# Performance work log

Measured on AMD Instinct MI355X. Metric: run time of the kernel, lower is better.

The kernel has to match this reference:

```python
import jax, jax.numpy as jnp
import numpy as np

B, P, N, H = 8, 12, 5000, 8
E = 50000
NB = 8
TD0, TD1 = 16, 64
MAX_STEPS = 500


def _proj(x, w1, b1, w2, b2):
    # Projection: Linear -> ReLU -> Linear
    return jax.nn.relu(x @ w1 + b1) @ w2 + b2


def _ln(x, w, b, eps=1e-5):
    # LayerNorm over last two dims [N, H] with affine params [N, H]
    m = jnp.mean(x, axis=(-2, -1), keepdims=True)
    v = jnp.mean((x - m) ** 2, axis=(-2, -1), keepdims=True)
    return (x - m) * jax.lax.rsqrt(v + eps) * w + b


def _time_table():
    # DiffTimeEmbedding buffer: [MAX_STEPS, 2*TD0]
    steps = jnp.arange(MAX_STEPS, dtype=jnp.float32)[:, None]
    dims = jnp.arange(TD0, dtype=jnp.float32)[None, :]
    e = steps * 10.0 ** (dims * 4.0 / TD0)
    return jnp.concatenate([jnp.sin(e), jnp.cos(e)], axis=1)


def setup_inputs() -> dict:
    key = jax.random.key(0)
    ks = jax.random.split(key, 40)
    rn = lambda k, s, sc=0.1: jax.random.normal(k, s, jnp.float32) * sc
    return {
        'x': jax.random.normal(ks[0], (B, P, N), jnp.float32),
        'cond': jax.random.normal(ks[1], (B, P, N, H), jnp.float32),
        'pos': jax.random.normal(ks[2], (N, H), jnp.float32),
        'time': jax.random.randint(ks[3], (B,), 0, MAX_STEPS),
        'edge_index': jax.random.randint(ks[4], (2, E), 0, N),
        'te_w1': rn(ks[5], (2 * TD0, TD1)), 'te_b1': rn(ks[6], (TD1,)),
        'te_w2': rn(ks[7], (TD1, TD1)), 'te_b2': rn(ks[8], (TD1,)),
        'in_w1': rn(ks[9], (1, H)), 'in_b1': rn(ks[10], (H,)),
        'in_w2': rn(ks[11], (H, H)), 'in_b2': rn(ks[12], (H,)),
        'pos_w1': rn(ks[13], (H, H)), 'pos_b1': rn(ks[14], (H,)),
        'pos_w2': rn(ks[15], (H, H)), 'pos_b2': rn(ks[16], (H,)),
        'attn': jax.random.normal(ks[17], (NB + 1, 1), jnp.float32),
        'bt_w1': rn(ks[18], (NB, TD1, H)), 'bt_b1': rn(ks[19], (NB, H)),
        'bt_w2': rn(ks[20], (NB, H, H)), 'bt_b2': rn(ks[21], (NB, H)),
        'bc_w1': rn(ks[22], (NB, H, H)), 'bc_b1': rn(ks[23], (NB, H)),
        'bc_w2': rn(ks[24], (NB, H, H)), 'bc_b2': rn(ks[25], (NB, H)),
        'gn_w': 1.0 + rn(ks[26], (NB, N, H), 0.05), 'gn_b': rn(ks[27], (NB, N, H), 0.05),
        'tn_w': 1.0 + rn(ks[28], (NB, N, H), 0.05), 'tn_b': rn(ks[29], (NB, N, H), 0.05),
        'cv_w': rn(ks[30], (NB, P, P)), 'cv_b': rn(ks[31], (NB, P)),
        'out_w1': rn(ks[32], (H, H)), 'out_b1': rn(ks[33], (H,)),
        'out_w2': rn(ks[34], (H, 1)), 'out_b2': rn(ks[35], (1,)),
    }


def _forward(x, cond, pos, te_w1, te_b1, te_w2, te_b2, in_w1, in_b1, in_w2, in_b2,
             pos_w1, pos_b1, pos_w2, pos_b2, attn, bt_w1, bt_b1, bt_w2, bt_b2,
             bc_w1, bc_b1, bc_w2, bc_b2, gn_w, gn_b, tn_w, tn_b, cv_w, cv_b,
             out_w1, out_b1, out_w2, out_b2, time, edge_index):
    # diffusion-time embedding -> [B, TD1]
    te = _time_table()[time]
    te = jax.nn.silu(te @ te_w1 + te_b1)
    te = jax.nn.silu(te @ te_w2 + te_b2)
    # input + positional projection -> [B, P, N, H]
    h = _proj(x[..., None], in_w1, in_b1, in_w2, in_b2)
    h = h + _proj(pos, pos_w1, pos_b1, pos_w2, pos_b2)
    # LGConv symmetric GCN norm (no self loops), shared across blocks
    src, dst = edge_index[0], edge_index[1]
    deg = jnp.zeros((N,), h.dtype).at[dst].add(1.0)
    dinv = jnp.where(deg > 0, 1.0 / jnp.sqrt(jnp.where(deg > 0, deg, 1.0)), 0.0)
    enorm = dinv[src] * dinv[dst]  # [E]
    skips = [h]
    for i in range(NB):
        t = _proj(te, bt_w1[i], bt_b1[i], bt_w2[i], bt_b2[i])[:, None, None, :]
        c = _proj(cond, bc_w1[i], bc_b1[i], bc_w2[i], bc_b2[i])
        h = _ln(h + c, gn_w[i], gn_b[i])
        # LGConv: gather -> scale -> scatter-add along node dim (-2)
        msg = h[:, :, src, :] * enorm[None, None, :, None]
        h = jnp.zeros_like(h).at[:, :, dst, :].add(msg)
        h = _ln(h + t, tn_w[i], tn_b[i])
        # 1x1 Conv2d over period channels
        h = jnp.einsum('bpnh,qp->bqnh', h, cv_w[i]) + cv_b[i][None, :, None, None]
        skips.append(h)
    s = jnp.stack(skips, axis=-1)  # [B, P, N, H, NB+1]
    a = jax.nn.softmax(attn, axis=0)  # [NB+1, 1]
    h = (s @ a)[..., 0]  # [B, P, N, H]
    return _proj(h, out_w1, out_b1, out_w2, out_b2)[..., 0]  # [B, P, N]


def reference(x, cond, pos, te_w1, te_b1, te_w2, te_b2, in_w1, in_b1, in_w2, in_b2,
              pos_w1, pos_b1, pos_w2, pos_b2, attn, bt_w1, bt_b1, bt_w2, bt_b2,
              bc_w1, bc_b1, bc_w2, bc_b2, gn_w, gn_b, tn_w, tn_b, cv_w, cv_b,
              out_w1, out_b1, out_w2, out_b2, time, edge_index):
    return _forward(x, cond, pos, te_w1, te_b1, te_w2, te_b2, in_w1, in_b1, in_w2, in_b2,
                    pos_w1, pos_b1, pos_w2, pos_b2, attn, bt_w1, bt_b1, bt_w2, bt_b2,
                    bc_w1, bc_b1, bc_w2, bc_b2, gn_w, gn_b, tn_w, tn_b, cv_w, cv_b,
                    out_w1, out_b1, out_w2, out_b2, time, edge_index)
```

## Files before the change

### kernel.cpp

```cpp
#include <hip/hip_runtime.h>
#include <math.h>

#define Bv 8
#define Pv 12
#define Nv 5000
#define Hv 8
#define Ev 50000
#define NBv 8
#define TD1v 64
#define NIMG (Bv * Pv)
#define BLKS_PER_IMG 20
#define CHUNKS1 10
#define ECAP 3072
#define IPT2 2
#define EU 8

typedef float f4v __attribute__((ext_vector_type(4)));

__device__ inline float4 nt_load4(const float* p) {
  f4v v = __builtin_nontemporal_load((const f4v*)p);
  return make_float4(v.x, v.y, v.z, v.w);
}
__device__ inline void nt_store4(float* p, float a, float b, float c, float d) {
  f4v v = {a, b, c, d};
  __builtin_nontemporal_store(v, (f4v*)p);
}

__device__ __constant__ float POW10Q[16] = {
  1.0f, 1.7782794100389228f, 3.1622776601683795f, 5.623413251903491f,
  10.0f, 17.78279410038923f, 31.622776601683793f, 56.23413251903491f,
  100.0f, 177.82794100389228f, 316.22776601683796f, 562.341325190349f,
  1000.0f, 1778.2794100389228f, 3162.2776601683795f, 5623.413251903491f
};

__global__ __launch_bounds__(512) void k_setup(
    const int* timei, const float* attn,
    const float* te_w1, const float* te_b1,
    const float* te_w2, const float* te_b2,
    const float* bt_w1, const float* bt_b1,
    const float* bt_w2, const float* bt_b2,
    float* t_all, float* a9) {
  __shared__ float te0[Bv][32];
  __shared__ float te1[Bv][64];
  __shared__ float te2[Bv][64];
  __shared__ float su[64][8];
  int t = threadIdx.x;
  if (t < 256) {
    int b = t >> 5, k = t & 31;
    int d = k & 15;
    float e = (float)timei[b] * POW10Q[d];
    te0[b][k] = (k < 16) ? (float)sin((double)e) : (float)cos((double)e);
  }
  __syncthreads();
  {
    int b = t >> 6, j = t & 63;
    float s = te_b1[j];
    for (int k = 0; k < 32; ++k) s += te0[b][k] * te_w1[k * 64 + j];
    te1[b][j] = s / (1.0f + expf(-s));
  }
  __syncthreads();
  {
    int b = t >> 6, j = t & 63;
    float s = te_b2[j];
    for (int k = 0; k < 64; ++k) s += te1[b][k] * te_w2[k * 64 + j];
    te2[b][j] = s / (1.0f + expf(-s));
  }
  __syncthreads();
  {
    int ib = t >> 3, j = t & 7;
    int i = ib >> 3, b = ib & 7;
    float s = bt_b1[i * Hv + j];
    for (int k = 0; k < TD1v; ++k) s += te2[b][k] * bt_w1[(i * TD1v + k) * Hv + j];
    su[ib][j] = fmaxf(s, 0.0f);
  }
  __syncthreads();
  {
    int ib = t >> 3, ch = t & 7;
    int i = ib >> 3, b = ib & 7;
    float s = bt_b2[i * Hv + ch];
    #pragma unroll
    for (int j = 0; j < 8; ++j) s += su[ib][j] * bt_w2[(i * Hv + j) * Hv + ch];
    t_all[(i * Bv + b) * Hv + ch] = s;
  }
  if (t == 0) {
    float m = attn[0];
    for (int i = 1; i < 9; ++i) m = fmaxf(m, attn[i]);
    float s = 0.f, ex[9];
    for (int i = 0; i < 9; ++i) { ex[i] = expf(attn[i] - m); s += ex[i]; }
    for (int i = 0; i < 9; ++i) a9[i] = ex[i] / s;
  }
}

__global__ void k_posp_zero(const float* pos, const float* pw1, const float* pb1,
                            const float* pw2, const float* pb2, float* posp,
                            float* deg, int* cursor, float* stats) {
  int n = blockIdx.x * blockDim.x + threadIdx.x;
  if (n < Nv) { deg[n] = 0.f; cursor[n] = 0; }
  if (n < NBv * 2 * NIMG * 2) stats[n] = 0.f;
  if (n >= Nv) return;
  const float4* pr = (const float4*)(pos + (size_t)n * Hv);
  float4 r0 = pr[0], r1 = pr[1];
  float x[8] = {r0.x, r0.y, r0.z, r0.w, r1.x, r1.y, r1.z, r1.w};
  float u[8];
  #pragma unroll
  for (int j = 0; j < 8; ++j) {
    float s = pb1[j];
    #pragma unroll
    for (int k = 0; k < 8; ++k) s += x[k] * pw1[k * 8 + j];
    u[j] = fmaxf(s, 0.f);
  }
  float o[8];
  #pragma unroll
  for (int ch = 0; ch < 8; ++ch) {
    float s = pb2[ch];
    #pragma unroll
    for (int j = 0; j < 8; ++j) s += u[j] * pw2[j * 8 + ch];
    o[ch] = s;
  }
  float4* po = (float4*)(posp + (size_t)n * Hv);
  po[0] = make_float4(o[0], o[1], o[2], o[3]);
  po[1] = make_float4(o[4], o[5], o[6], o[7]);
}

__global__ void k_deg(const int* eidx, float* deg) {
  int e = blockIdx.x * blockDim.x + threadIdx.x;
  if (e < Ev) atomicAdd(&deg[eidx[Ev + e]], 1.0f);
}

__global__ __launch_bounds__(1024) void k_scan(const float* deg, float* dinv,
                                               int* row_ptr) {
  __shared__ int wsum[16];
  __shared__ int base_s;
  int t = threadIdx.x;
  int lane = t & 63, wid = t >> 6;
  if (t == 0) { base_s = 0; row_ptr[0] = 0; }
  __syncthreads();
  for (int c = 0; c < 5; ++c) {
    int i = c * 1024 + t;
    float dv = (i < Nv) ? deg[i] : 0.f;
    if (i < Nv)
      dinv[i] = dv > 0.f ? (float)(1.0 / sqrt((double)dv)) : 0.f;
    int v = (int)(dv + 0.5f);
    int s = v;
    #pragma unroll
    for (int off = 1; off < 64; off <<= 1) {
      int up = __shfl_up(s, off, 64);
      if (lane >= off) s += up;
    }
    if (lane == 63) wsum[wid] = s;
    __syncthreads();
    if (wid == 0 && lane < 16) {
      int ws = wsum[lane];
      #pragma unroll
      for (int off = 1; off < 16; off <<= 1) {
        int up = __shfl_up(ws, off, 64);
        if (lane >= off) ws += up;
      }
      wsum[lane] = ws;
    }
    __syncthreads();
    int wbase = (wid > 0) ? wsum[wid - 1] : 0;
    int incl = base_s + wbase + s;
    if (i < Nv) row_ptr[i + 1] = incl;
    __syncthreads();
    if (t == 1023) base_s = incl;
    __syncthreads();
  }
}

__global__ void k_csr(const int* eidx, const float* dinv, const int* row_ptr,
                      int* cursor, float2* epack) {
  int e = blockIdx.x * blockDim.x + threadIdx.x;
  if (e >= Ev) return;
  int s = eidx[e], d = eidx[Ev + e];
  int slot = atomicAdd(&cursor[d], 1);
  int pos = row_ptr[d] + slot;
  epack[pos] = make_float2(__int_as_float(s), dinv[s] * dinv[d]);
}

__global__ __launch_bounds__(256) void k_gwb(
    const int* __restrict__ row_ptr, const float2* __restrict__ epack,
    const float* __restrict__ gn_w, const float* __restrict__ gn_b,
    float* __restrict__ Gw, float* __restrict__ Gb) {
  int id = blockIdx.x * 256 + threadIdx.x;
  if (id >= NBv * Nv) return;
  int i = id / Nv, n = id % Nv;
  const float* gw = gn_w + (size_t)i * Nv * Hv;
  const float* gb = gn_b + (size_t)i * Nv * Hv;
  float aw[8] = {0,0,0,0,0,0,0,0}, ab[8] = {0,0,0,0,0,0,0,0};
  int e0 = row_ptr[n], e1 = row_ptr[n + 1];
  for (int e = e0; e < e1; ++e) {
    float2 ep = epack[e];
    int s = __float_as_int(ep.x);
    float w = ep.y;
    const float4* wr = (const float4*)(gw + (size_t)s * Hv);
    const float4* br = (const float4*)(gb + (size_t)s * Hv);
    float4 w0 = wr[0], w1 = wr[1], b0 = br[0], b1 = br[1];
    aw[0] += w * w0.x; aw[1] += w * w0.y; aw[2] += w * w0.z; aw[3] += w * w0.w;
    aw[4] += w * w1.x; aw[5] += w * w1.y; aw[6] += w * w1.z; aw[7] += w * w1.w;
    ab[0] += w * b0.x; ab[1] += w * b0.y; ab[2] += w * b0.z; ab[3] += w * b0.w;
    ab[4] += w * b1.x; ab[5] += w * b1.y; ab[6] += w * b1.z; ab[7] += w * b1.w;
  }
  float4* wo = (float4*)(Gw + (size_t)id * Hv);
  wo[0] = make_float4(aw[0], aw[1], aw[2], aw[3]);
  wo[1] = make_float4(aw[4], aw[5], aw[6], aw[7]);
  float4* bo = (float4*)(Gb + (size_t)id * Hv);
  bo[0] = make_float4(ab[0], ab[1], ab[2], ab[3]);
  bo[1] = make_float4(ab[4], ab[5], ab[6], ab[7]);
}

__device__ inline void partial_to_stats(float s1, float s2, float* stats_g) {
  #pragma unroll
  for (int off = 32; off > 0; off >>= 1) {
    s1 += __shfl_down(s1, off, 64);
    s2 += __shfl_down(s2, off, 64);
  }
  __shared__ float r1[4], r2[4];
  int wid = threadIdx.x >> 6, lane = threadIdx.x & 63;
  if (lane == 0) { r1[wid] = s1; r2[wid] = s2; }
  __syncthreads();
  if (threadIdx.x == 0) {
    float a = r1[0] + r1[1] + r1[2] + r1[3];
    float b = r2[0] + r2[1] + r2[2] + r2[3];
    atomicAdd(&stats_g[0], a);
    atomicAdd(&stats_g[1], b);
  }
  __syncthreads();
}

__global__ __launch_bounds__(256) void k_stage1(
    const float* __restrict__ h, const float* __restrict__ cond,
    const float* w1, const float* b1, const float* w2, const float* b2,
    const float* __restrict__ gnw,
    float* __restrict__ vt, float* stats1) {
  __shared__ float lw1[64], lw2[64], lb1[8], lb2[8];
  int t = threadIdx.x;
  if (t < 64) lw1[t] = w1[t];
  else if (t < 128) lw2[t - 64] = w2[t - 64];
  else if (t < 136) lb1[t - 128] = b1[t - 128];
  else if (t < 144) lb2[t - 136] = b2[t - 136];
  __syncthreads();
  int xcd = blockIdx.x & 7;
  int local = blockIdx.x >> 3;
  int g = xcd * 12 + local / CHUNKS1;
  int chunk = local % CHUNKS1;
  int n0 = chunk * 512 + t;
  float s1 = 0.f, s2 = 0.f;
  #pragma unroll
  for (int r = 0; r < 2; ++r) {
    int n = n0 + r * 256;
    if (n < Nv) {
      size_t row = ((size_t)g * Nv + n) * Hv;
      float4 c0 = nt_load4(cond + row);
      float4 c1 = nt_load4(cond + row + 4);
      float xc[8] = {c0.x, c0.y, c0.z, c0.w, c1.x, c1.y, c1.z, c1.w};
      float u[8];
      #pragma unroll
      for (int j = 0; j < 8; ++j) {
        float s = lb1[j];
        #pragma unroll
        for (int k = 0; k < 8; ++k) s += xc[k] * lw1[k * 8 + j];
        u[j] = fmaxf(s, 0.f);
      }
      const float4* hr = (const float4*)(h + row);
      float4 h0 = hr[0], h1 = hr[1];
      float hv[8] = {h0.x, h0.y, h0.z, h0.w, h1.x, h1.y, h1.z, h1.w};
      const float4* gr = (const float4*)(gnw + (size_t)n * Hv);
      float4 g0 = gr[0], g1 = gr[1];
      float gv[8] = {g0.x, g0.y, g0.z, g0.w, g1.x, g1.y, g1.z, g1.w};
      float o[8];
      #pragma unroll
      for (int ch = 0; ch < 8; ++ch) {
        float s = lb2[ch];
        #pragma unroll
        for (int j = 0; j < 8; ++j) s += u[j] * lw2[j * 8 + ch];
        float val = s + hv[ch];
        s1 += val; s2 += val * val;
        o[ch] = val * gv[ch];
      }
      float4* vo = (float4*)(vt + row);
      vo[0] = make_float4(o[0], o[1], o[2], o[3]);
      vo[1] = make_float4(o[4], o[5], o[6], o[7]);
    }
  }
  partial_to_stats(s1, s2, stats1 + (size_t)g * 2);
}

__global__ __launch_bounds__(256) void k_stage1_init(
    const float* __restrict__ x, const float* __restrict__ posp,
    const float* iw1, const float* ib1, const float* iw2, const float* ib2,
    const float* __restrict__ cond,
    const float* w1, const float* b1, const float* w2, const float* b2,
    const float* __restrict__ gnw, const float* __restrict__ a9,
    float* __restrict__ acc,
    float* __restrict__ vt, float* stats1) {
  __shared__ float lw1[64], lw2[64], lb1[8], lb2[8];
  __shared__ float li1[8], li2[64], lib1[8], lib2[8];
  int t = threadIdx.x;
  if (t < 64) lw1[t] = w1[t];
  else if (t < 128) lw2[t - 64] = w2[t - 64];
  else if (t < 136) lb1[t - 128] = b1[t - 128];
  else if (t < 144) lb2[t - 136] = b2[t - 136];
  else if (t < 152) li1[t - 144] = iw1[t - 144];
  else if (t < 216) li2[t - 152] = iw2[t - 152];
  else if (t < 224) lib1[t - 216] = ib1[t - 216];
  else if (t < 232) lib2[t - 224] = ib2[t - 224];
  __syncthreads();
  int xcd = blockIdx.x & 7;
  int local = blockIdx.x >> 3;
  int g = xcd * 12 + local / BLKS_PER_IMG;
  int chunk = local % BLKS_PER_IMG;
  int n = chunk * 256 + t;
  float s1 = 0.f, s2 = 0.f;
  if (n < Nv) {
    size_t row = ((size_t)g * Nv + n) * Hv;
    float xv = __builtin_nontemporal_load(x + (size_t)g * Nv + n);
    float ui[8];
    #pragma unroll
    for (int j = 0; j < 8; ++j) ui[j] = fmaxf(xv * li1[j] + lib1[j], 0.f);
    const float4* pp = (const float4*)(posp + (size_t)n * Hv);
    float4 p0 = pp[0], p1 = pp[1];
    float pv[8] = {p0.x, p0.y, p0.z, p0.w, p1.x, p1.y, p1.z, p1.w};
    float hv[8];
    #pragma unroll
    for (int ch = 0; ch < 8; ++ch) {
      float s = lib2[ch];
      #pragma unroll
      for (int j = 0; j < 8; ++j) s += ui[j] * li2[j * 8 + ch];
      hv[ch] = s + pv[ch];
    }
    float a0 = a9[0];
    float4* ar = (float4*)(acc + row);
    ar[0] = make_float4(a0 * hv[0], a0 * hv[1], a0 * hv[2], a0 * hv[3]);
    ar[1] = make_float4(a0 * hv[4], a0 * hv[5], a0 * hv[6], a0 * hv[7]);
    float4 c0 = nt_load4(cond + row);
    float4 c1 = nt_load4(cond + row + 4);
    float xc[8] = {c0.x, c0.y, c0.z, c0.w, c1.x, c1.y, c1.z, c1.w};
    float u[8];
    #pragma unroll
    for (int j = 0; j < 8; ++j) {
      float s = lb1[j];
      #pragma unroll
      for (int k = 0; k < 8; ++k) s += xc[k] * lw1[k * 8 + j];
      u[j] = fmaxf(s, 0.f);
    }
    const float4* gr = (const float4*)(gnw + (size_t)n * Hv);
    float4 g0 = gr[0], g1 = gr[1];
    float gv[8] = {g0.x, g0.y, g0.z, g0.w, g1.x, g1.y, g1.z, g1.w};
    float o[8];
    #pragma unroll
    for (int ch = 0; ch < 8; ++ch) {
      float s = lb2[ch];
      #pragma unroll
      for (int j = 0; j < 8; ++j) s += u[j] * lw2[j * 8 + ch];
      float val = s + hv[ch];
      s1 += val; s2 += val * val;
      o[ch] = val * gv[ch];
    }
    float4* vo = (float4*)(vt + row);
    vo[0] = make_float4(o[0], o[1], o[2], o[3]);
    vo[1] = make_float4(o[4], o[5], o[6], o[7]);
  }
  partial_to_stats(s1, s2, stats1 + (size_t)g * 2);
}

__global__ __launch_bounds__(256) void k_stage2(
    const float* __restrict__ vt, float* __restrict__ v2,
    const int* __restrict__ row_ptr, const float2* __restrict__ epack,
    const float* __restrict__ Gw, const float* __restrict__ Gb,
    const float* __restrict__ stats1, float* stats2,
    const float* __restrict__ tvec) {
  __shared__ float2 se[ECAP];
  int t = threadIdx.x;
  int b = blockIdx.x & 7;
  int local = blockIdx.x >> 3;
  int pair = local % 6;
  int chunk = local / 6;
  int g0 = b * Pv + pair * IPT2;
  int nb0 = chunk * 256;
  int nb1 = nb0 + 256; if (nb1 > Nv) nb1 = Nv;
  int eb0 = row_ptr[nb0];
  int eb1 = row_ptr[nb1];
  int cnt = eb1 - eb0;
  const float2* eps;
  int ebase;
  if (cnt <= ECAP) {
    for (int k = t; k < cnt; k += 256) se[k] = epack[eb0 + k];
    eps = se; ebase = eb0;
  } else {
    eps = epack; ebase = 0;
  }
  __syncthreads();
  float mean[IPT2], rstd[IPT2], mrs[IPT2];
  #pragma unroll
  for (int j = 0; j < IPT2; ++j) {
    float m  = stats1[(g0 + j) * 2]     * (1.f / 40000.f);
    float m2 = stats1[(g0 + j) * 2 + 1] * (1.f / 40000.f);
    float var = m2 - m * m;
    mean[j] = m;
    rstd[j] = (float)(1.0 / sqrt((double)var + 1e-5));
    mrs[j]  = m * rstd[j];
  }
  int n = nb0 + t;
  float s1a[IPT2], s2a[IPT2];
  #pragma unroll
  for (int j = 0; j < IPT2; ++j) { s1a[j] = 0.f; s2a[j] = 0.f; }
  if (n < Nv) {
    const float* vt0 = vt + (size_t)(g0 + 0) * Nv * Hv;
    const float* vt1 = vt + (size_t)(g0 + 1) * Nv * Hv;
    float a[IPT2][8];
    #pragma unroll
    for (int j = 0; j < IPT2; ++j)
      #pragma unroll
      for (int ch = 0; ch < 8; ++ch) a[j][ch] = 0.f;
    int e0 = row_ptr[n] - ebase, e1 = row_ptr[n + 1] - ebase;
    int e = e0;
    for (; e + EU <= e1; e += EU) {
      float2 pp[EU];
      float4 A0[EU], B0[EU], A1[EU], B1[EU];
      #pragma unroll
      for (int k = 0; k < EU; ++k) pp[k] = eps[e + k];
      #pragma unroll
      for (int k = 0; k < EU; ++k) {
        size_t so = (size_t)__float_as_int(pp[k].x) * Hv;
        const float4* r0 = (const float4*)(vt0 + so);
        const float4* r1 = (const float4*)(vt1 + so);
        A0[k] = r0[0]; B0[k] = r0[1];
        A1[k] = r1[0]; B1[k] = r1[1];
      }
      #pragma unroll
      for (int k = 0; k < EU; ++k) {
        float w = pp[k].y;
        a[0][0] += w * A0[k].x; a[0][1] += w * A0[k].y;
        a[0][2] += w * A0[k].z; a[0][3] += w * A0[k].w;
        a[0][4] += w * B0[k].x; a[0][5] += w * B0[k].y;
        a[0][6] += w * B0[k].z; a[0][7] += w * B0[k].w;
        a[1][0] += w * A1[k].x; a[1][1] += w * A1[k].y;
        a[1][2] += w * A1[k].z; a[1][3] += w * A1[k].w;
        a[1][4] += w * B1[k].x; a[1][5] += w * B1[k].y;
        a[1][6] += w * B1[k].z; a[1][7] += w * B1[k].w;
      }
    }
    for (; e < e1; ++e) {
      float2 ep = eps[e];
      float w = ep.y;
      size_t so = (size_t)__float_as_int(ep.x) * Hv;
      const float4* r0 = (const float4*)(vt0 + so);
      const float4* r1 = (const float4*)(vt1 + so);
      float4 xa = r0[0], xb = r0[1];
      float4 ya = r1[0], yb = r1[1];
      a[0][0] += w*xa.x; a[0][1] += w*xa.y; a[0][2] += w*xa.z; a[0][3] += w*xa.w;
      a[0][4] += w*xb.x; a[0][5] += w*xb.y; a[0][6] += w*xb.z; a[0][7] += w*xb.w;
      a[1][0] += w*ya.x; a[1][1] += w*ya.y; a[1][2] += w*ya.z; a[1][3] += w*ya.w;
      a[1][4] += w*yb.x; a[1][5] += w*yb.y; a[1][6] += w*yb.z; a[1][7] += w*yb.w;
    }
    size_t noff = (size_t)n * Hv;
    const float4* wr = (const float4*)(Gw + noff);
    const float4* br = (const float4*)(Gb + noff);
    float4 w0 = wr[0], w1 = wr[1], b0 = br[0], b1 = br[1];
    float gw8[8] = {w0.x, w0.y, w0.z, w0.w, w1.x, w1.y, w1.z, w1.w};
    float gb8[8] = {b0.x, b0.y, b0.z, b0.w, b1.x, b1.y, b1.z, b1.w};
    float tl[8];
    {
      const float4* tr = (const float4*)(tvec + b * Hv);
      float4 t0 = tr[0], t1 = tr[1];
      tl[0] = t0.x; tl[1] = t0.y; tl[2] = t0.z; tl[3] = t0.w;
      tl[4] = t1.x; tl[5] = t1.y; tl[6] = t1.z; tl[7] = t1.w;
    }
    #pragma unroll
    for (int j = 0; j < IPT2; ++j) {
      float o[8];
      #pragma unroll
      for (int ch = 0; ch < 8; ++ch) {
        float val = rstd[j] * a[j][ch] - mrs[j] * gw8[ch] + gb8[ch] + tl[ch];
        o[ch] = val;
        s1a[j] += val; s2a[j] += val * val;
      }
      float* vo = v2 + (size_t)(g0 + j) * Nv * Hv + noff;
      nt_store4(vo,     o[0], o[1], o[2], o[3]);
      nt_store4(vo + 4, o[4], o[5], o[6], o[7]);
    }
  }
  #pragma unroll
  for (int j = 0; j < IPT2; ++j)
    partial_to_stats(s1a[j], s2a[j], stats2 + (size_t)(g0 + j) * 2);
}

__global__ __launch_bounds__(256) void k_stage3(
    float* __restrict__ v2, float* __restrict__ acc,
    const float* __restrict__ stats2,
    const float* __restrict__ tnw, const float* __restrict__ tnb,
    const float* __restrict__ cw, const float* __restrict__ cb,
    const float* __restrict__ a9, int iblk,
    const float* __restrict__ ow1, const float* __restrict__ ob1,
    const float* __restrict__ ow2, const float* __restrict__ ob2,
    float* __restrict__ out) {
  __shared__ float scw[144], scb[12], smean[12], srstd[12];
  __shared__ float sow1[64], sob1[8], sow2[8], sob2[1];
  int t = threadIdx.x;
  int b = blockIdx.x & 7;
  int chunk = blockIdx.x >> 3;
  bool last = (iblk == NBv - 1);
  if (t < 144) scw[t] = cw[t];
  else if (t < 156) scb[t - 144] = cb[t - 144];
  else if (t < 168) {
    int p = t - 156;
    int g = b * Pv + p;
    float mean = stats2[g * 2]     * (1.f / 40000.f);
    float m2   = stats2[g * 2 + 1] * (1.f / 40000.f);
    float var  = m2 - mean * mean;
    smean[p] = mean;
    srstd[p] = (float)(1.0 / sqrt((double)var + 1e-5));
  } else if (last) {
    if (t < 232) sow1[t - 168] = ow1[t - 168];
    else if (t < 240) sob1[t - 232] = ob1[t - 232];
    else if (t < 248) sow2[t - 240] = ow2[t - 240];
    else if (t == 248) sob2[0] = ob2[0];
  }
  __syncthreads();
  int idx = chunk * 256 + t;
  if (idx >= Nv * 2) return;
  int n = idx >> 1, c4 = idx & 1;
  size_t noff = (size_t)n * Hv + c4 * 4;
  const float4 w4 = nt_load4(tnw + noff);
  const float4 b4 = nt_load4(tnb + noff);
  size_t strideP = (size_t)Nv * Hv;
  size_t base = (size_t)b * Pv * strideP + noff;
  float4 in[12];
  #pragma unroll
  for (int p = 0; p < 12; ++p) {
    float4 v = nt_load4(v2 + base + p * strideP);
    float mean = smean[p], rstd = srstd[p];
    in[p].x = (v.x - mean) * rstd * w4.x + b4.x;
    in[p].y = (v.y - mean) * rstd * w4.y + b4.y;
    in[p].z = (v.z - mean) * rstd * w4.z + b4.z;
    in[p].w = (v.w - mean) * rstd * w4.w + b4.w;
  }
  float ai = a9[iblk + 1];
  #pragma unroll
  for (int q = 0; q < 12; ++q) {
    float4 o = make_float4(scb[q], scb[q], scb[q], scb[q]);
    #pragma unroll
    for (int p = 0; p < 12; ++p) {
      float c = scw[q * 12 + p];
      o.x += c * in[p].x; o.y += c * in[p].y;
      o.z += c * in[p].z; o.w += c * in[p].w;
    }
    size_t off = base + q * strideP;
    float4* ap = (float4*)(acc + off);
    float4 av = *ap;
    float n0 = av.x + ai * o.x, n1 = av.y + ai * o.y;
    float n2 = av.z + ai * o.z, n3 = av.w + ai * o.w;
    if (!last) {
      *(float4*)(v2 + off) = o;
      *ap = make_float4(n0, n1, n2, n3);
    } else {
      float e0 = __shfl_xor(n0, 1, 64);
      float e1 = __shfl_xor(n1, 1, 64);
      float e2 = __shfl_xor(n2, 1, 64);
      float e3 = __shfl_xor(n3, 1, 64);
      float a8[8];
      if (c4 == 0) {
        a8[0] = n0; a8[1] = n1; a8[2] = n2; a8[3] = n3;
        a8[4] = e0; a8[5] = e1; a8[6] = e2; a8[7] = e3;
      } else {
        a8[0] = e0; a8[1] = e1; a8[2] = e2; a8[3] = e3;
        a8[4] = n0; a8[5] = n1; a8[6] = n2; a8[7] = n3;
      }
      if (c4 == 0) {
        float oo = sob2[0];
        #pragma unroll
        for (int j = 0; j < 8; ++j) {
          float s = sob1[j];
          #pragma unroll
          for (int k = 0; k < 8; ++k) s += a8[k] * sow1[k * 8 + j];
          oo += fmaxf(s, 0.f) * sow2[j];
        }
        out[((size_t)b * Pv + q) * Nv + n] = oo;
      }
    }
  }
}

extern "C" void kernel_launch(void* const* d_in, const int* in_sizes, int n_in,
                              void* d_out, int out_size, void* d_ws, size_t ws_size,
                              hipStream_t stream) {
  const float* x      = (const float*)d_in[0];
  const float* cond   = (const float*)d_in[1];
  const float* pos    = (const float*)d_in[2];
  const int*   timei  = (const int*)  d_in[3];
  const int*   eidx   = (const int*)  d_in[4];
  const float* te_w1  = (const float*)d_in[5];
  const float* te_b1  = (const float*)d_in[6];
  const float* te_w2  = (const float*)d_in[7];
  const float* te_b2  = (const float*)d_in[8];
  const float* in_w1  = (const float*)d_in[9];
  const float* in_b1  = (const float*)d_in[10];
  const float* in_w2  = (const float*)d_in[11];
  const float* in_b2  = (const float*)d_in[12];
  const float* pos_w1 = (const float*)d_in[13];
  const float* pos_b1 = (const float*)d_in[14];
  const float* pos_w2 = (const float*)d_in[15];
  const float* pos_b2 = (const float*)d_in[16];
  const float* attn   = (const float*)d_in[17];
  const float* bt_w1  = (const float*)d_in[18];
  const float* bt_b1  = (const float*)d_in[19];
  const float* bt_w2  = (const float*)d_in[20];
  const float* bt_b2  = (const float*)d_in[21];
  const float* bc_w1  = (const float*)d_in[22];
  const float* bc_b1  = (const float*)d_in[23];
  const float* bc_w2  = (const float*)d_in[24];
  const float* bc_b2  = (const float*)d_in[25];
  const float* gn_w   = (const float*)d_in[26];
  const float* gn_b   = (const float*)d_in[27];
  const float* tn_w   = (const float*)d_in[28];
  const float* tn_b   = (const float*)d_in[29];
  const float* cv_w   = (const float*)d_in[30];
  const float* cv_b   = (const float*)d_in[31];
  const float* out_w1 = (const float*)d_in[32];
  const float* out_b1 = (const float*)d_in[33];
  const float* out_w2 = (const float*)d_in[34];
  const float* out_b2 = (const float*)d_in[35];
  float* out = (float*)d_out;

  const size_t HSZ = (size_t)Bv * Pv * Nv * Hv;
  float* ws    = (float*)d_ws;
  float* X     = ws;
  float* Y     = X + HSZ;
  float* acc   = Y + HSZ;
  float* posp  = acc + HSZ;
  float* deg   = posp + Nv * Hv;
  float* dinv  = deg + Nv;
  float* epack = dinv + Nv;
  float* t_all = epack + 2 * Ev;
  float* a9    = t_all + NBv * Bv * Hv;
  float* stats = a9 + 16;
  float* Gw    = stats + NBv * 2 * NIMG * 2;
  float* Gb    = Gw + NBv * Nv * Hv;
  int* row_ptr = (int*)(Gb + NBv * Nv * Hv);
  int* cursor  = row_ptr + Nv + 8;

  k_setup<<<1, 512, 0, stream>>>(timei, attn, te_w1, te_b1, te_w2, te_b2,
                                 bt_w1, bt_b1, bt_w2, bt_b2, t_all, a9);
  k_posp_zero<<<(Nv + 255) / 256, 256, 0, stream>>>(
      pos, pos_w1, pos_b1, pos_w2, pos_b2, posp, deg, cursor, stats);
  k_deg<<<(Ev + 255) / 256, 256, 0, stream>>>(eidx, deg);
  k_scan<<<1, 1024, 0, stream>>>(deg, dinv, row_ptr);
  k_csr<<<(Ev + 255) / 256, 256, 0, stream>>>(eidx, dinv, row_ptr, cursor, (float2*)epack);
  k_gwb<<<(NBv * Nv + 255) / 256, 256, 0, stream>>>(
      row_ptr, (const float2*)epack, gn_w, gn_b, Gw, Gb);

  for (int i = 0; i < NBv; ++i) {
    float* st1 = stats + (size_t)(i * 2 + 0) * NIMG * 2;
    float* st2 = stats + (size_t)(i * 2 + 1) * NIMG * 2;
    if (i == 0) {
      k_stage1_init<<<NIMG * BLKS_PER_IMG, 256, 0, stream>>>(
          x, posp, in_w1, in_b1, in_w2, in_b2,
          cond, bc_w1, bc_b1, bc_w2, bc_b2,
          gn_w, a9, acc, Y, st1);
    } else {
      k_stage1<<<8 * 12 * CHUNKS1, 256, 0, stream>>>(
          X, cond,
          bc_w1 + i * 64, bc_b1 + i * 8, bc_w2 + i * 64, bc_b2 + i * 8,
          gn_w + (size_t)i * Nv * Hv,
          Y, st1);
    }
    k_stage2<<<8 * 6 * BLKS_PER_IMG, 256, 0, stream>>>(
        Y, X, row_ptr, (const float2*)epack,
        Gw + (size_t)i * Nv * Hv, Gb + (size_t)i * Nv * Hv,
        st1, st2, t_all + i * Bv * Hv);
    k_stage3<<<8 * 40, 256, 0, stream>>>(
        X, acc, st2,
        tn_w + (size_t)i * Nv * Hv, tn_b + (size_t)i * Nv * Hv,
        cv_w + i * 144, cv_b + i * 12, a9, i,
        out_w1, out_b1, out_w2, out_b2, out);
  }
}
```

Before: 553.8 us.

## Split stage3 output channels across two blocks and unroll the gwb edge loop

Stage3 now launches twice as many blocks, and each block computes half of the twelve output period channels. This raises parallelism on a grid that previously had fewer blocks than the GPU has compute units. Because the two halves would race on an in-place write, stage3 now writes its output to a separate buffer, and stage1 updates that buffer in place. The cost is that every block still reads all twelve input channels, which doubles the stage3 input reads. The one-time k_gwb edge gather is also unrolled by four so that more independent loads are in flight.

After: 544.8 us. About the same (-1.6%).

```diff
diff --git a/kernel.cpp b/kernel.cpp
--- a/kernel.cpp
+++ b/kernel.cpp
@@ -189,7 +189,43 @@
   const float* gb = gn_b + (size_t)i * Nv * Hv;
   float aw[8] = {0,0,0,0,0,0,0,0}, ab[8] = {0,0,0,0,0,0,0,0};
   int e0 = row_ptr[n], e1 = row_ptr[n + 1];
-  for (int e = e0; e < e1; ++e) {
+  int e = e0;
+  for (; e + 4 <= e1; e += 4) {
+    float2 p0 = epack[e], p1 = epack[e+1], p2 = epack[e+2], p3 = epack[e+3];
+    size_t s0 = (size_t)__float_as_int(p0.x) * Hv;
+    size_t s1 = (size_t)__float_as_int(p1.x) * Hv;
+    size_t s2 = (size_t)__float_as_int(p2.x) * Hv;
+    size_t s3 = (size_t)__float_as_int(p3.x) * Hv;
+    const float4* w0p = (const float4*)(gw + s0);
+    const float4* w1p = (const float4*)(gw + s1);
+    const float4* w2p = (const float4*)(gw + s2);
+    const float4* w3p = (const float4*)(gw + s3);
+    const float4* b0p = (const float4*)(gb + s0);
+    const float4* b1p = (const float4*)(gb + s1);
+    const float4* b2p = (const float4*)(gb + s2);
+    const float4* b3p = (const float4*)(gb + s3);
+    float4 wa0 = w0p[0], wb0 = w0p[1], wa1 = w1p[0], wb1 = w1p[1];
+    float4 wa2 = w2p[0], wb2 = w2p[1], wa3 = w3p[0], wb3 = w3p[1];
+    float4 ba0 = b0p[0], bb0 = b0p[1], ba1 = b1p[0], bb1 = b1p[1];
+    float4 ba2 = b2p[0], bb2 = b2p[1], ba3 = b3p[0], bb3 = b3p[1];
+    aw[0] += p0.y*wa0.x + p1.y*wa1.x + p2.y*wa2.x + p3.y*wa3.x;
+    aw[1] += p0.y*wa0.y + p1.y*wa1.y + p2.y*wa2.y + p3.y*wa3.y;
+    aw[2] += p0.y*wa0.z + p1.y*wa1.z + p2.y*wa2.z + p3.y*wa3.z;
+    aw[3] += p0.y*wa0.w + p1.y*wa1.w + p2.y*wa2.w + p3.y*wa3.w;
+    aw[4] += p0.y*wb0.x + p1.y*wb1.x + p2.y*wb2.x + p3.y*wb3.x;
+    aw[5] += p0.y*wb0.y + p1.y*wb1.y + p2.y*wb2.y + p3.y*wb3.y;
+    aw[6] += p0.y*wb0.z + p1.y*wb1.z + p2.y*wb2.z + p3.y*wb3.z;
+    aw[7] += p0.y*wb0.w + p1.y*wb1.w + p2.y*wb2.w + p3.y*wb3.w;
+    ab[0] += p0.y*ba0.x + p1.y*ba1.x + p2.y*ba2.x + p3.y*ba3.x;
+    ab[1] += p0.y*ba0.y + p1.y*ba1.y + p2.y*ba2.y + p3.y*ba3.y;
+    ab[2] += p0.y*ba0.z + p1.y*ba1.z + p2.y*ba2.z + p3.y*ba3.z;
+    ab[3] += p0.y*ba0.w + p1.y*ba1.w + p2.y*ba2.w + p3.y*ba3.w;
+    ab[4] += p0.y*bb0.x + p1.y*bb1.x + p2.y*bb2.x + p3.y*bb3.x;
+    ab[5] += p0.y*bb0.y + p1.y*bb1.y + p2.y*bb2.y + p3.y*bb3.y;
+    ab[6] += p0.y*bb0.z + p1.y*bb1.z + p2.y*bb2.z + p3.y*bb3.z;
+    ab[7] += p0.y*bb0.w + p1.y*bb1.w + p2.y*bb2.w + p3.y*bb3.w;
+  }
+  for (; e < e1; ++e) {
     float2 ep = epack[e];
     int s = __float_as_int(ep.x);
     float w = ep.y;
@@ -229,10 +265,10 @@
 }
 
 __global__ __launch_bounds__(256) void k_stage1(
-    const float* __restrict__ h, const float* __restrict__ cond,
+    float* __restrict__ hv_buf, const float* __restrict__ cond,
     const float* w1, const float* b1, const float* w2, const float* b2,
     const float* __restrict__ gnw,
-    float* __restrict__ vt, float* stats1) {
+    float* stats1) {
   __shared__ float lw1[64], lw2[64], lb1[8], lb2[8];
   int t = threadIdx.x;
   if (t < 64) lw1[t] = w1[t];
@@ -262,7 +298,7 @@
         for (int k = 0; k < 8; ++k) s += xc[k] * lw1[k * 8 + j];
         u[j] = fmaxf(s, 0.f);
       }
-      const float4* hr = (const float4*)(h + row);
+      const float4* hr = (const float4*)(hv_buf + row);
       float4 h0 = hr[0], h1 = hr[1];
       float hv[8] = {h0.x, h0.y, h0.z, h0.w, h1.x, h1.y, h1.z, h1.w};
       const float4* gr = (const float4*)(gnw + (size_t)n * Hv);
@@ -278,7 +314,7 @@
         s1 += val; s2 += val * val;
         o[ch] = val * gv[ch];
       }
-      float4* vo = (float4*)(vt + row);
+      float4* vo = (float4*)(hv_buf + row);
       vo[0] = make_float4(o[0], o[1], o[2], o[3]);
       vo[1] = make_float4(o[4], o[5], o[6], o[7]);
     }
@@ -487,7 +523,8 @@
 }
 
 __global__ __launch_bounds__(256) void k_stage3(
-    float* __restrict__ v2, float* __restrict__ acc,
+    const float* __restrict__ v2, float* __restrict__ hout,
+    float* __restrict__ acc,
     const float* __restrict__ stats2,
     const float* __restrict__ tnw, const float* __restrict__ tnb,
     const float* __restrict__ cw, const float* __restrict__ cb,
@@ -499,7 +536,9 @@
   __shared__ float sow1[64], sob1[8], sow2[8], sob2[1];
   int t = threadIdx.x;
   int b = blockIdx.x & 7;
-  int chunk = blockIdx.x >> 3;
+  int local = blockIdx.x >> 3;
+  int qh = local & 1;
+  int chunk = local >> 1;
   bool last = (iblk == NBv - 1);
   if (t < 144) scw[t] = cw[t];
   else if (t < 156) scb[t - 144] = cb[t - 144];
@@ -537,8 +576,10 @@
     in[p].w = (v.w - mean) * rstd * w4.w + b4.w;
   }
   float ai = a9[iblk + 1];
-  #pragma unroll
-  for (int q = 0; q < 12; ++q) {
+  int q0 = qh * 6;
+  #pragma unroll
+  for (int qi = 0; qi < 6; ++qi) {
+    int q = q0 + qi;
     float4 o = make_float4(scb[q], scb[q], scb[q], scb[q]);
     #pragma unroll
     for (int p = 0; p < 12; ++p) {
@@ -552,7 +593,7 @@
     float n0 = av.x + ai * o.x, n1 = av.y + ai * o.y;
     float n2 = av.z + ai * o.z, n3 = av.w + ai * o.w;
     if (!last) {
-      *(float4*)(v2 + off) = o;
+      *(float4*)(hout + off) = o;
       *ap = make_float4(n0, n1, n2, n3);
     } else {
       float e0 = __shfl_xor(n0, 1, 64);
@@ -660,17 +701,17 @@
           gn_w, a9, acc, Y, st1);
     } else {
       k_stage1<<<8 * 12 * CHUNKS1, 256, 0, stream>>>(
-          X, cond,
+          Y, cond,
           bc_w1 + i * 64, bc_b1 + i * 8, bc_w2 + i * 64, bc_b2 + i * 8,
           gn_w + (size_t)i * Nv * Hv,
-          Y, st1);
+          st1);
     }
     k_stage2<<<8 * 6 * BLKS_PER_IMG, 256, 0, stream>>>(
         Y, X, row_ptr, (const float2*)epack,
         Gw + (size_t)i * Nv * Hv, Gb + (size_t)i * Nv * Hv,
         st1, st2, t_all + i * Bv * Hv);
-    k_stage3<<<8 * 40, 256, 0, stream>>>(
-        X, acc, st2,
+    k_stage3<<<8 * 40 * 2, 256, 0, stream>>>(
+        X, Y, acc, st2,
         tn_w + (size_t)i * Nv * Hv, tn_b + (size_t)i * Nv * Hv,
         cv_w + i * 144, cv_b + i * 12, a9, i,
         out_w1, out_b1, out_w2, out_b2, out);
```
